# Performance work log

Hardware: AMD Instinct MI355X
Metric: run time of the kernel (lower is better)

## Reference

```python
import jax, jax.numpy as jnp
import numpy as np

N_NODES = 50000
N_EDGES = 800000
D_IN = 128
D_HID = 128   # initlial_net_sizes[-1]
D_GC = 128    # gc_out
D_OUT = 256   # feats_out


def setup_inputs() -> dict:
    key = jax.random.key(0)
    ks = jax.random.split(key, 8)
    feats = jax.random.normal(ks[0], (N_NODES, D_IN), dtype=jnp.float32)
    edges = jax.random.randint(ks[1], (2, N_EDGES), 0, N_NODES, dtype=jnp.int64)
    batch = jnp.sort(jax.random.randint(ks[2], (N_NODES,), 0, 64, dtype=jnp.int64))
    s = 0.05
    W1 = jax.random.normal(ks[3], (D_IN, D_HID), dtype=jnp.float32) * s
    b1 = jnp.zeros((D_HID,), dtype=jnp.float32)
    Wg = jax.random.normal(ks[4], (D_HID, D_GC), dtype=jnp.float32) * s
    bg = jnp.zeros((D_GC,), dtype=jnp.float32)
    W2 = jax.random.normal(ks[5], (D_HID + D_GC, D_OUT), dtype=jnp.float32) * s
    b2 = jnp.zeros((D_OUT,), dtype=jnp.float32)
    return {"feats": feats, "edges": edges, "batch": batch,
            "W1": W1, "b1": b1, "Wg": Wg, "bg": bg, "W2": W2, "b2": b2}


def _gcn_conv(x, edges, Wg, bg):
    # PyG GCNConv: linear -> add self-loops -> sym degree norm -> scatter-add -> bias
    n = x.shape[0]
    x = x @ Wg                                   # [N, D_GC]
    loop = jnp.arange(n, dtype=edges.dtype)
    src = jnp.concatenate([edges[0], loop])      # message source (x_j)
    dst = jnp.concatenate([edges[1], loop])      # aggregation target
    deg = jax.ops.segment_sum(jnp.ones_like(dst, dtype=x.dtype), dst, num_segments=n)
    dinv = jnp.where(deg > 0, jax.lax.rsqrt(deg), 0.0)
    norm = dinv[src] * dinv[dst]                 # [E+N]
    msg = x[src] * norm[:, None]                 # [E+N, D_GC]
    out = jax.ops.segment_sum(msg, dst, num_segments=n)
    return out + bg


def reference(feats, edges, batch, W1, b1, Wg, bg, W2, b2):
    nfeats = feats @ W1 + b1                     # fcnn (single Linear, no activation)
    gc_feats = _gcn_conv(nfeats, edges, Wg, bg)  # GCNConv
    combined = jnp.concatenate([nfeats, gc_feats], axis=1) @ W2 + b2
    return (combined, edges, batch)
```

## Files before the change

kernel.cpp:

```cpp
#include <hip/hip_runtime.h>
#include <hip/hip_bf16.h>
#include <stdint.h>


#define NND 50000
#define NE  800000

typedef unsigned int u32;
typedef unsigned short u16;
typedef unsigned long long u64;
typedef short bf16x8 __attribute__((ext_vector_type(8)));
typedef float f32x4  __attribute__((ext_vector_type(4)));

#define OFF_CSR  12800000
#define OFF_RNK  13200000
#define OFF_ROW  13600000
#define OFF_DEG  13700004
#define OFF_DINV 13750004
#define OFF_WPK2 13800004
#define OFF_WPK1 13832772
#define OFF_WPKG 13840964
#define OFF_BSUM 13849156
#define OFF_BOFF 13849412
#define OFF_FLG  13849668

__device__ __forceinline__ float bf_lo(u32 u) { return __uint_as_float(u << 16); }
__device__ __forceinline__ float bf_hi(u32 u) { return __uint_as_float(u & 0xFFFF0000u); }
__device__ __forceinline__ unsigned short f2b(float f) {
    __hip_bfloat16 h = __float2bfloat16(f);
    return *(unsigned short*)&h;
}

__device__ __forceinline__ int probe_isbf_par(const u32* p, int stride, int lane) {
    u32 v = p[lane * stride];
    u32 e = (v >> 7) & 0xFFu;
    u64 m = __ballot(e >= 90u && e <= 150u);
    return (__popcll(m) >= 40) ? 1 : 0;
}
__device__ __forceinline__ int probe_intfmt_par(const u32* p, int base, int stride, int lane) {
    int i = lane & 31;
    bool lo = lane < 32;
    u32 a = p[base + i * stride];
    u32 b = p[base + i * stride + 1];
    u32 e1 = (a >> 7) & 0xFFu;
    int small = __popcll(__ballot(lo && a < 50000u))
              + __popcll(__ballot(lo && b < 50000u));
    int oddz  = __popcll(__ballot(lo && b == 0u));
    int bfe   = __popcll(__ballot(lo && e1 >= 110u && e1 <= 145u));
    return (small >= 56) ? ((oddz >= 31) ? 1 : 0) : ((bfe >= 20) ? 3 : 2);
}

__device__ __forceinline__ int iread(const void* p, int fmt, int idx) {
    switch (fmt) {
        case 0:  return ((const int*)p)[idx];
        case 1:  return ((const int*)p)[2 * idx];
        case 2:  return (int)(((const float*)p)[idx] + 0.5f);
        default: return (int)(__bfloat162float(((const __hip_bfloat16*)p)[idx]) + 0.5f);
    }
}
__device__ __forceinline__ float fread_pass(const void* p, int fmt, int idx) {
    switch (fmt) {
        case 0:  return (float)((const int*)p)[idx];
        case 1:  return (float)((const int*)p)[2 * idx];
        case 2:  return ((const float*)p)[idx];
        default: return __bfloat162float(((const __hip_bfloat16*)p)[idx]);
    }
}
__device__ __forceinline__ float rdf(const void* p, int idx, int isbf) {
    return isbf ? __bfloat162float(((const __hip_bfloat16*)p)[idx])
                : ((const float*)p)[idx];
}
__device__ __forceinline__ float rdbias(const void* p, int idx) {
    return __bfloat162float(((const __hip_bfloat16*)p)[idx]);
}

__global__ void k_flags(const u32* feats, const u32* W1, const u32* Wg,
                        const u32* W2, const u32* ew, const u32* bw,
                        int* __restrict__ flags)
{
    int w = threadIdx.x >> 6, lane = threadIdx.x & 63;
    if      (w == 0) { int r = probe_isbf_par(feats, 997, lane);        if (lane == 0) flags[0] = r; }
    else if (w == 1) { int r = probe_isbf_par(W1, 127, lane);           if (lane == 0) flags[3] = r; }
    else if (w == 2) { int r = probe_isbf_par(Wg, 127, lane);           if (lane == 0) flags[4] = r; }
    else if (w == 3) { int r = probe_isbf_par(W2, 509, lane);           if (lane == 0) flags[5] = r; }
    else if (w == 4) { int r = probe_intfmt_par(ew, 0, 24992, lane);    if (lane == 0) flags[1] = r; }
    else if (w == 5) { int r = probe_intfmt_par(bw, 20000, 156, lane);  if (lane == 0) flags[2] = r; }
}

__global__ __launch_bounds__(256) void k_degrank(const void* edges,
                                                 const int* __restrict__ flags,
                                                 int* __restrict__ deg,
                                                 u16* __restrict__ rank16)
{
    int fmt = flags[1];
    int e = blockIdx.x * 256 + threadIdx.x;
    if (e < NE) {
        int s = iread(edges, fmt, e);
        int d = iread(edges, fmt, NE + e);
        if ((u32)s < (u32)NND && (u32)d < (u32)NND) {
            int r = atomicAdd(&deg[d], 1);
            rank16[e] = (u16)r;
        }
    }
}

__global__ __launch_bounds__(256) void k_scan1(const int* __restrict__ deg,
                                               int* __restrict__ bsum)
{
    __shared__ int part[256];
    int t = threadIdx.x, idx = blockIdx.x * 256 + t;
    part[t] = (idx < NND) ? deg[idx] : 0;
    __syncthreads();
    for (int off = 128; off >= 1; off >>= 1) {
        if (t < off) part[t] += part[t + off];
        __syncthreads();
    }
    if (t == 0) bsum[blockIdx.x] = part[0];
}

__global__ __launch_bounds__(256) void k_scan2(const int* __restrict__ bsum,
                                               int* __restrict__ boff,
                                               int* __restrict__ row_start)
{
    __shared__ int part[256];
    int t = threadIdx.x;
    int v = (t < 196) ? bsum[t] : 0;
    part[t] = v;
    __syncthreads();
    for (int off = 1; off < 256; off <<= 1) {
        int x = (t >= off) ? part[t - off] : 0;
        __syncthreads();
        part[t] += x;
        __syncthreads();
    }
    if (t < 196) boff[t] = part[t] - v;
    if (t == 255) row_start[NND] = part[255];
}

__global__ __launch_bounds__(256) void k_scan3(const int* __restrict__ deg,
                                               const int* __restrict__ boff,
                                               int* __restrict__ row_start,
                                               float* __restrict__ dinv)
{
    __shared__ int part[256];
    int t = threadIdx.x, idx = blockIdx.x * 256 + t;
    int dv = (idx < NND) ? deg[idx] : 0;
    part[t] = dv;
    __syncthreads();
    for (int off = 1; off < 256; off <<= 1) {
        int x = (t >= off) ? part[t - off] : 0;
        __syncthreads();
        part[t] += x;
        __syncthreads();
    }
    if (idx < NND) {
        int rs = boff[blockIdx.x] + part[t] - dv;
        row_start[idx] = rs;
        dinv[idx] = rsqrtf((float)(dv + 1));
    }
}

__global__ __launch_bounds__(256) void k_place(const void* edges,
                                               const int* __restrict__ flags,
                                               const int* __restrict__ row_start,
                                               const u16* __restrict__ rank16,
                                               u16* __restrict__ csr16)
{
    int fmt = flags[1];
    int e = blockIdx.x * 256 + threadIdx.x;
    if (e < NE) {
        int s = iread(edges, fmt, e);
        int d = iread(edges, fmt, NE + e);
        if ((u32)s < (u32)NND && (u32)d < (u32)NND) {
            int pos = row_start[d] + (int)rank16[e];
            csr16[pos] = (u16)s;
        }
    }
}

__global__ __launch_bounds__(256) void k_pw128(const void* W, const int* flg,
                                               unsigned short* __restrict__ Wpk)
{
    int wbf = *flg;
    int idx = blockIdx.x * 256 + threadIdx.x;
    if (idx < 16384) {
        int j = idx & 7, l = (idx >> 3) & 63, nt = (idx >> 9) & 7, kk = (idx >> 12) & 3;
        int k = kk * 32 + ((l >> 4) & 3) * 8 + j;
        int n = nt * 16 + (l & 15);
        Wpk[idx] = f2b(rdf(W, k * 128 + n, wbf));
    }
}

__global__ __launch_bounds__(256) void k_pw2(const void* W2, const int* flg,
                                             unsigned short* __restrict__ Wpk)
{
    int wbf = *flg;
    int idx = blockIdx.x * 256 + threadIdx.x;
    if (idx < 65536) {
        int j = idx & 7, l = (idx >> 3) & 63, nt = (idx >> 9) & 15, kk = idx >> 13;
        int k = kk * 32 + ((l >> 4) & 3) * 8 + j;
        int n = nt * 16 + (l & 15);
        Wpk[idx] = f2b(rdf(W2, k * 256 + n, wbf));
    }
}

__global__ __launch_bounds__(256) void k_nf(
    const void* feats, const int* __restrict__ flags,
    const u32* __restrict__ Wpk1, const void* b1, float* __restrict__ out, int M)
{
    __shared__ u32 sApk[2048];
    int tid = threadIdx.x;
    int fbf = flags[0];
    int row0 = blockIdx.x * 32;

    if (fbf) {
        const u32* fw = (const u32*)feats;
        for (int idx = tid; idx < 2048; idx += 256) {
            int jp = idx & 3, l = (idx >> 2) & 63, kk = (idx >> 8) & 3, mt = (idx >> 10) & 1;
            int m = mt * 16 + (l & 15);
            int k0 = kk * 32 + ((l >> 4) & 3) * 8 + jp * 2;
            int row = row0 + m;
            sApk[idx] = (row < M) ? fw[(size_t)row * 64 + (k0 >> 1)] : 0u;
        }
    } else {
        const float* ff = (const float*)feats;
        for (int idx = tid; idx < 2048; idx += 256) {
            int jp = idx & 3, l = (idx >> 2) & 63, kk = (idx >> 8) & 3, mt = (idx >> 10) & 1;
            int m = mt * 16 + (l & 15);
            int k0 = kk * 32 + ((l >> 4) & 3) * 8 + jp * 2;
            int row = row0 + m;
            u32 u = 0u;
            if (row < M) {
                float f0 = ff[(size_t)row * 128 + k0];
                float f1 = ff[(size_t)row * 128 + k0 + 1];
                u = ((u32)f2b(f1) << 16) | (u32)f2b(f0);
            }
            sApk[idx] = u;
        }
    }
    __syncthreads();

    int w = tid >> 6, lane = tid & 63;
    f32x4 acc[2][2];
#pragma unroll
    for (int mt = 0; mt < 2; ++mt)
#pragma unroll
        for (int t = 0; t < 2; ++t) acc[mt][t] = (f32x4){0.f, 0.f, 0.f, 0.f};

    for (int kk = 0; kk < 4; ++kk) {
        union { uint4 u; bf16x8 h; } ca0, ca1;
        ca0.u = *(const uint4*)&sApk[(kk * 64 + lane) * 4];
        ca1.u = *(const uint4*)&sApk[((4 + kk) * 64 + lane) * 4];
#pragma unroll
        for (int t = 0; t < 2; ++t) {
            int nt = w * 2 + t;
            union { uint4 u; bf16x8 h; } cb;
            cb.u = *(const uint4*)&Wpk1[((kk * 8 + nt) * 64 + lane) * 4];
            acc[0][t] = __builtin_amdgcn_mfma_f32_16x16x32_bf16(ca0.h, cb.h, acc[0][t], 0, 0, 0);
            acc[1][t] = __builtin_amdgcn_mfma_f32_16x16x32_bf16(ca1.h, cb.h, acc[1][t], 0, 0, 0);
        }
    }

    unsigned short* o16 = (unsigned short*)out;
    int q = lane >> 4, cn = lane & 15;
#pragma unroll
    for (int mt = 0; mt < 2; ++mt)
#pragma unroll
        for (int t = 0; t < 2; ++t) {
            int col = (w * 2 + t) * 16 + cn;
            float bb = rdbias(b1, col);
#pragma unroll
            for (int r = 0; r < 4; ++r) {
                int row = row0 + mt * 16 + q * 4 + r;
                if (row < M) o16[(size_t)row * 512 + col] = f2b(acc[mt][t][r] + bb);
            }
        }
}

__global__ __launch_bounds__(256) void k_xp(
    const u32* __restrict__ Wpkg, const float* __restrict__ dinv,
    float* __restrict__ out, int M)
{
    __shared__ u32 sApk[2048];
    int tid = threadIdx.x;
    int row0 = blockIdx.x * 32;
    const u32* uw = (const u32*)out;

    for (int idx = tid; idx < 2048; idx += 256) {
        int jp = idx & 3, l = (idx >> 2) & 63, kk = (idx >> 8) & 3, mt = (idx >> 10) & 1;
        int m = mt * 16 + (l & 15);
        int k0 = kk * 32 + ((l >> 4) & 3) * 8 + jp * 2;
        int row = row0 + m;
        sApk[idx] = (row < M) ? uw[(size_t)row * 256 + (k0 >> 1)] : 0u;
    }
    __syncthreads();

    int w = tid >> 6, lane = tid & 63;
    f32x4 acc[2][2];
#pragma unroll
    for (int mt = 0; mt < 2; ++mt)
#pragma unroll
        for (int t = 0; t < 2; ++t) acc[mt][t] = (f32x4){0.f, 0.f, 0.f, 0.f};

    for (int kk = 0; kk < 4; ++kk) {
        union { uint4 u; bf16x8 h; } ca0, ca1;
        ca0.u = *(const uint4*)&sApk[(kk * 64 + lane) * 4];
        ca1.u = *(const uint4*)&sApk[((4 + kk) * 64 + lane) * 4];
#pragma unroll
        for (int t = 0; t < 2; ++t) {
            int nt = w * 2 + t;
            union { uint4 u; bf16x8 h; } cb;
            cb.u = *(const uint4*)&Wpkg[((kk * 8 + nt) * 64 + lane) * 4];
            acc[0][t] = __builtin_amdgcn_mfma_f32_16x16x32_bf16(ca0.h, cb.h, acc[0][t], 0, 0, 0);
            acc[1][t] = __builtin_amdgcn_mfma_f32_16x16x32_bf16(ca1.h, cb.h, acc[1][t], 0, 0, 0);
        }
    }

    unsigned short* o16 = (unsigned short*)out;
    int q = lane >> 4, cn = lane & 15;
#pragma unroll
    for (int mt = 0; mt < 2; ++mt)
#pragma unroll
        for (int t = 0; t < 2; ++t) {
            int col = (w * 2 + t) * 16 + cn;
#pragma unroll
            for (int r = 0; r < 4; ++r) {
                int row = row0 + mt * 16 + q * 4 + r;
                if (row < M)
                    o16[(size_t)row * 512 + 256 + col] = f2b(acc[mt][t][r] * dinv[row]);
            }
        }
}

__global__ __launch_bounds__(256) void k_gather(
    const u16* __restrict__ csr16, const int* __restrict__ row_start,
    const float* __restrict__ dinv, const void* bg, u32* __restrict__ uw)
{
    int gt = blockIdx.x * 256 + threadIdx.x;
    int node = gt >> 6, l = gt & 63;
    if (node >= NND) return;
    int beg = row_start[node], end = row_start[node + 1];

    u32 us = uw[(size_t)node * 256 + 128 + l];
    float di = dinv[node];
    float bg0 = rdbias(bg, 2 * l);
    float bg1 = rdbias(bg, 2 * l + 1);

    float a0 = 0.f, a1 = 0.f;
    float c0 = 0.f, c1 = 0.f;
    int e0 = end - 1;
    for (int i = beg; i < end; i += 8) {
        int j1 = i + 1, j2 = i + 2, j3 = i + 3;
        int j4 = i + 4, j5 = i + 5, j6 = i + 6, j7 = i + 7;
        int s0 = csr16[i];
        int s1 = csr16[j1 < e0 ? j1 : e0];
        int s2 = csr16[j2 < e0 ? j2 : e0];
        int s3 = csr16[j3 < e0 ? j3 : e0];
        int s4 = csr16[j4 < e0 ? j4 : e0];
        int s5 = csr16[j5 < e0 ? j5 : e0];
        int s6 = csr16[j6 < e0 ? j6 : e0];
        int s7 = csr16[j7 < e0 ? j7 : e0];
        u32 u0 = uw[(size_t)s0 * 256 + 128 + l];
        u32 u1 = uw[(size_t)s1 * 256 + 128 + l];
        u32 u2 = uw[(size_t)s2 * 256 + 128 + l];
        u32 u3 = uw[(size_t)s3 * 256 + 128 + l];
        u32 u4 = uw[(size_t)s4 * 256 + 128 + l];
        u32 u5 = uw[(size_t)s5 * 256 + 128 + l];
        u32 u6 = uw[(size_t)s6 * 256 + 128 + l];
        u32 u7 = uw[(size_t)s7 * 256 + 128 + l];
        float w1 = (j1 <= e0) ? 1.f : 0.f;
        float w2 = (j2 <= e0) ? 1.f : 0.f;
        float w3 = (j3 <= e0) ? 1.f : 0.f;
        float w4 = (j4 <= e0) ? 1.f : 0.f;
        float w5 = (j5 <= e0) ? 1.f : 0.f;
        float w6 = (j6 <= e0) ? 1.f : 0.f;
        float w7 = (j7 <= e0) ? 1.f : 0.f;
        a0 += bf_lo(u0);            a1 += bf_hi(u0);
        c0 = fmaf(w1, bf_lo(u1), c0); c1 = fmaf(w1, bf_hi(u1), c1);
        a0 = fmaf(w2, bf_lo(u2), a0); a1 = fmaf(w2, bf_hi(u2), a1);
        c0 = fmaf(w3, bf_lo(u3), c0); c1 = fmaf(w3, bf_hi(u3), c1);
        a0 = fmaf(w4, bf_lo(u4), a0); a1 = fmaf(w4, bf_hi(u4), a1);
        c0 = fmaf(w5, bf_lo(u5), c0); c1 = fmaf(w5, bf_hi(u5), c1);
        a0 = fmaf(w6, bf_lo(u6), a0); a1 = fmaf(w6, bf_hi(u6), a1);
        c0 = fmaf(w7, bf_lo(u7), c0); c1 = fmaf(w7, bf_hi(u7), c1);
    }
    a0 += c0; a1 += c1;
    float g0 = di * (a0 + bf_lo(us)) + bg0;
    float g1 = di * (a1 + bf_hi(us)) + bg1;
    uw[(size_t)node * 256 + 192 + l] = ((u32)f2b(g1) << 16) | (u32)f2b(g0);
}

__global__ __launch_bounds__(256) void k_final(
    const u32* __restrict__ Wpk, const void* b2, float* __restrict__ out, int M)
{
    __shared__ u32 sApk[4096];
    int tid = threadIdx.x;
    int row0 = blockIdx.x * 32;
    const u32* uw = (const u32*)out;

    for (int idx = tid; idx < 4096; idx += 256) {
        int jp = idx & 3, l = (idx >> 2) & 63, kk = (idx >> 8) & 7, mt = (idx >> 11) & 1;
        int m = mt * 16 + (l & 15);
        int k0 = kk * 32 + ((l >> 4) & 3) * 8 + jp * 2;
        int row = row0 + m;
        u32 u = 0u;
        if (row < M) {
            if (kk < 4) u = uw[(size_t)row * 256 + (k0 >> 1)];
            else        u = uw[(size_t)row * 256 + 192 + ((k0 - 128) >> 1)];
        }
        sApk[idx] = u;
    }
    __syncthreads();

    int w = tid >> 6, lane = tid & 63;
    f32x4 acc[2][4];
#pragma unroll
    for (int mt = 0; mt < 2; ++mt)
#pragma unroll
        for (int t = 0; t < 4; ++t) acc[mt][t] = (f32x4){0.f, 0.f, 0.f, 0.f};

    for (int kk = 0; kk < 8; ++kk) {
        union { uint4 u; bf16x8 h; } ca0, ca1;
        ca0.u = *(const uint4*)&sApk[(kk * 64 + lane) * 4];
        ca1.u = *(const uint4*)&sApk[((8 + kk) * 64 + lane) * 4];
#pragma unroll
        for (int t = 0; t < 4; ++t) {
            int nt = w * 4 + t;
            union { uint4 u; bf16x8 h; } cb;
            cb.u = *(const uint4*)&Wpk[((size_t)(kk * 16 + nt) * 64 + lane) * 4];
            acc[0][t] = __builtin_amdgcn_mfma_f32_16x16x32_bf16(ca0.h, cb.h, acc[0][t], 0, 0, 0);
            acc[1][t] = __builtin_amdgcn_mfma_f32_16x16x32_bf16(ca1.h, cb.h, acc[1][t], 0, 0, 0);
        }
    }

    int q = lane >> 4, cn = lane & 15;
#pragma unroll
    for (int mt = 0; mt < 2; ++mt)
#pragma unroll
        for (int t = 0; t < 4; ++t) {
            int col = w * 64 + t * 16 + cn;
            float bb = rdbias(b2, col);
#pragma unroll
            for (int r = 0; r < 4; ++r) {
                int row = row0 + mt * 16 + q * 4 + r;
                if (row < M) {
                    float v = acc[mt][t][r] + bb;
                    if (!(fabsf(v) < 900.f)) v = (v == v) ? copysignf(900.f, v) : 0.f;
                    out[(size_t)row * 256 + col] = v;
                }
            }
        }
}

__global__ __launch_bounds__(256) void k_tail(
    const void* edges, const void* batch, const int* __restrict__ flags,
    float* __restrict__ out)
{
    int f0 = flags[1], f1 = flags[2];
    int i = blockIdx.x * 256 + threadIdx.x;
    if (i < 2 * NE) {
        out[(size_t)NND * 256 + i] = fread_pass(edges, f0, i);
    } else if (i < 2 * NE + NND) {
        out[(size_t)NND * 256 + i] = fread_pass(batch, f1, i - 2 * NE);
    }
}

extern "C" void kernel_launch(void* const* d_in, const int* in_sizes, int n_in,
                              void* d_out, int out_size, void* d_ws, size_t ws_size,
                              hipStream_t stream)
{
    int i_feats = -1, i_edges = -1, i_batch = -1, i_W1 = -1, i_Wg = -1,
        i_W2 = -1, i_b1 = -1, i_bg = -1, i_b2 = -1;
    for (int i = 0; i < n_in; ++i) {
        int s = in_sizes[i];
        if      (s == 6400000) i_feats = i;
        else if (s == 1600000) i_edges = i;
        else if (s == 50000)   i_batch = i;
        else if (s == 65536)   i_W2 = i;
        else if (s == 256)     i_b2 = i;
        else if (s == 16384)   { if (i_W1 < 0) i_W1 = i; else i_Wg = i; }
        else if (s == 128)     { if (i_b1 < 0) i_b1 = i; else i_bg = i; }
    }
    if (i_feats < 0 || i_edges < 0 || i_batch < 0 || i_W1 < 0 || i_Wg < 0 ||
        i_W2 < 0 || i_b1 < 0 || i_bg < 0 || i_b2 < 0) {
        i_feats = 0; i_edges = 1; i_batch = 2; i_W1 = 3; i_b1 = 4;
        i_Wg = 5; i_bg = 6; i_W2 = 7; i_b2 = 8;
    }
    const void* feats = d_in[i_feats];
    const void* edges = d_in[i_edges];
    const void* batch = d_in[i_batch];
    const void* W1 = d_in[i_W1];
    const void* b1 = d_in[i_b1];
    const void* Wg = d_in[i_Wg];
    const void* bg = d_in[i_bg];
    const void* W2 = d_in[i_W2];
    const void* b2 = d_in[i_b2];

    float* out = (float*)d_out;
    u16*   csr16     = (u16*)  (out + OFF_CSR);
    u16*   rank16    = (u16*)  (out + OFF_RNK);
    int*   row_start = (int*)  (out + OFF_ROW);
    int*   deg       = (int*)  (out + OFF_DEG);
    float* dinv      = (float*)(out + OFF_DINV);
    unsigned short* Wpk2 = (unsigned short*)(out + OFF_WPK2);
    unsigned short* Wpk1 = (unsigned short*)(out + OFF_WPK1);
    unsigned short* Wpkg = (unsigned short*)(out + OFF_WPKG);
    int*   bsum  = (int*)(out + OFF_BSUM);
    int*   boff  = (int*)(out + OFF_BOFF);
    int*   flags = (int*)(out + OFF_FLG);

    hipMemsetAsync(deg, 0, 200000, stream);
    k_flags  <<<1,     384, 0, stream>>>((const u32*)feats, (const u32*)W1,
                                         (const u32*)Wg, (const u32*)W2,
                                         (const u32*)edges, (const u32*)batch, flags);
    k_degrank<<<3125,  256, 0, stream>>>(edges, flags, deg, rank16);
    k_scan1  <<<196,   256, 0, stream>>>(deg, bsum);
    k_scan2  <<<1,     256, 0, stream>>>(bsum, boff, row_start);
    k_scan3  <<<196,   256, 0, stream>>>(deg, boff, row_start, dinv);
    k_place  <<<3125,  256, 0, stream>>>(edges, flags, row_start, rank16, csr16);
    k_pw128  <<<64,    256, 0, stream>>>(W1, flags + 3, Wpk1);
    k_pw128  <<<64,    256, 0, stream>>>(Wg, flags + 4, Wpkg);
    k_pw2    <<<256,   256, 0, stream>>>(W2, flags + 5, Wpk2);
    k_nf     <<<1563,  256, 0, stream>>>(feats, flags, (const u32*)Wpk1, b1, out, NND);
    k_xp     <<<1563,  256, 0, stream>>>((const u32*)Wpkg, dinv, out, NND);
    k_gather <<<12500, 256, 0, stream>>>(csr16, row_start, dinv, bg, (u32*)out);
    k_final  <<<1563,  256, 0, stream>>>((const u32*)Wpk2, b2, out, NND);
    k_tail   <<<6446,  256, 0, stream>>>(edges, batch, flags, out);
}
```

Baseline: 241.9 us.

## Fuse preprocessing kernels and move dinv scaling into gather

Cuts the launch chain from 14 kernels to 7. Degree counting and weight packing become one launch, the block scan is merged with the node-feature and Wg GEMMs (the Wg GEMM reads nfeats from shared memory instead of global), and the scan2 and scan3 stages are merged. The flags kernel is dropped, so each block now re-probes the input formats. Because the dinv source scaling moves from the xp epilogue into the gather loop, this removes a dependency and the redundant global reload of nfeats. In exchange, each gathered edge now does an extra random dinv load and every block runs extra probe work.

```diff
diff --git a/kernel.cpp b/kernel.cpp
--- a/kernel.cpp
+++ b/kernel.cpp
@@ -21,8 +21,6 @@
 #define OFF_WPK1 13832772
 #define OFF_WPKG 13840964
 #define OFF_BSUM 13849156
-#define OFF_BOFF 13849412
-#define OFF_FLG  13849668
 
 __device__ __forceinline__ float bf_lo(u32 u) { return __uint_as_float(u << 16); }
 __device__ __forceinline__ float bf_hi(u32 u) { return __uint_as_float(u & 0xFFFF0000u); }
@@ -74,144 +72,75 @@
     return __bfloat162float(((const __hip_bfloat16*)p)[idx]);
 }
 
-__global__ void k_flags(const u32* feats, const u32* W1, const u32* Wg,
-                        const u32* W2, const u32* ew, const u32* bw,
-                        int* __restrict__ flags)
-{
-    int w = threadIdx.x >> 6, lane = threadIdx.x & 63;
-    if      (w == 0) { int r = probe_isbf_par(feats, 997, lane);        if (lane == 0) flags[0] = r; }
-    else if (w == 1) { int r = probe_isbf_par(W1, 127, lane);           if (lane == 0) flags[3] = r; }
-    else if (w == 2) { int r = probe_isbf_par(Wg, 127, lane);           if (lane == 0) flags[4] = r; }
-    else if (w == 3) { int r = probe_isbf_par(W2, 509, lane);           if (lane == 0) flags[5] = r; }
-    else if (w == 4) { int r = probe_intfmt_par(ew, 0, 24992, lane);    if (lane == 0) flags[1] = r; }
-    else if (w == 5) { int r = probe_intfmt_par(bw, 20000, 156, lane);  if (lane == 0) flags[2] = r; }
-}
-
-__global__ __launch_bounds__(256) void k_degrank(const void* edges,
-                                                 const int* __restrict__ flags,
-                                                 int* __restrict__ deg,
-                                                 u16* __restrict__ rank16)
-{
-    int fmt = flags[1];
-    int e = blockIdx.x * 256 + threadIdx.x;
-    if (e < NE) {
-        int s = iread(edges, fmt, e);
-        int d = iread(edges, fmt, NE + e);
-        if ((u32)s < (u32)NND && (u32)d < (u32)NND) {
-            int r = atomicAdd(&deg[d], 1);
-            rank16[e] = (u16)r;
-        }
-    }
-}
-
-__global__ __launch_bounds__(256) void k_scan1(const int* __restrict__ deg,
-                                               int* __restrict__ bsum)
-{
-    __shared__ int part[256];
-    int t = threadIdx.x, idx = blockIdx.x * 256 + t;
-    part[t] = (idx < NND) ? deg[idx] : 0;
-    __syncthreads();
-    for (int off = 128; off >= 1; off >>= 1) {
-        if (t < off) part[t] += part[t + off];
-        __syncthreads();
-    }
-    if (t == 0) bsum[blockIdx.x] = part[0];
-}
-
-__global__ __launch_bounds__(256) void k_scan2(const int* __restrict__ bsum,
-                                               int* __restrict__ boff,
-                                               int* __restrict__ row_start)
-{
-    __shared__ int part[256];
-    int t = threadIdx.x;
-    int v = (t < 196) ? bsum[t] : 0;
-    part[t] = v;
-    __syncthreads();
-    for (int off = 1; off < 256; off <<= 1) {
-        int x = (t >= off) ? part[t - off] : 0;
-        __syncthreads();
-        part[t] += x;
-        __syncthreads();
-    }
-    if (t < 196) boff[t] = part[t] - v;
-    if (t == 255) row_start[NND] = part[255];
-}
-
-__global__ __launch_bounds__(256) void k_scan3(const int* __restrict__ deg,
-                                               const int* __restrict__ boff,
-                                               int* __restrict__ row_start,
-                                               float* __restrict__ dinv)
-{
-    __shared__ int part[256];
-    int t = threadIdx.x, idx = blockIdx.x * 256 + t;
-    int dv = (idx < NND) ? deg[idx] : 0;
-    part[t] = dv;
-    __syncthreads();
-    for (int off = 1; off < 256; off <<= 1) {
-        int x = (t >= off) ? part[t - off] : 0;
-        __syncthreads();
-        part[t] += x;
-        __syncthreads();
-    }
-    if (idx < NND) {
-        int rs = boff[blockIdx.x] + part[t] - dv;
-        row_start[idx] = rs;
-        dinv[idx] = rsqrtf((float)(dv + 1));
-    }
-}
-
-__global__ __launch_bounds__(256) void k_place(const void* edges,
-                                               const int* __restrict__ flags,
-                                               const int* __restrict__ row_start,
-                                               const u16* __restrict__ rank16,
-                                               u16* __restrict__ csr16)
-{
-    int fmt = flags[1];
-    int e = blockIdx.x * 256 + threadIdx.x;
-    if (e < NE) {
-        int s = iread(edges, fmt, e);
-        int d = iread(edges, fmt, NE + e);
-        if ((u32)s < (u32)NND && (u32)d < (u32)NND) {
-            int pos = row_start[d] + (int)rank16[e];
-            csr16[pos] = (u16)s;
-        }
-    }
-}
-
-__global__ __launch_bounds__(256) void k_pw128(const void* W, const int* flg,
-                                               unsigned short* __restrict__ Wpk)
-{
-    int wbf = *flg;
-    int idx = blockIdx.x * 256 + threadIdx.x;
-    if (idx < 16384) {
+__global__ __launch_bounds__(256) void k_degpack(
+    const void* edges, const void* W1, const void* Wg, const void* W2,
+    int* __restrict__ deg, u16* __restrict__ rank16,
+    u16* __restrict__ Wpk1, u16* __restrict__ Wpkg, u16* __restrict__ Wpk2)
+{
+    int b = blockIdx.x, tid = threadIdx.x, lane = tid & 63;
+    if (b < 3125) {
+        int fmt = probe_intfmt_par((const u32*)edges, 0, 24992, lane);
+        int e = b * 256 + tid;
+        if (e < NE) {
+            int s = iread(edges, fmt, e);
+            int d = iread(edges, fmt, NE + e);
+            if ((u32)s < (u32)NND && (u32)d < (u32)NND) {
+                int r = atomicAdd(&deg[d], 1);
+                rank16[e] = (u16)r;
+            }
+        }
+    } else if (b < 3189) {
+        int wbf = probe_isbf_par((const u32*)W1, 127, lane);
+        int idx = (b - 3125) * 256 + tid;
         int j = idx & 7, l = (idx >> 3) & 63, nt = (idx >> 9) & 7, kk = (idx >> 12) & 3;
         int k = kk * 32 + ((l >> 4) & 3) * 8 + j;
         int n = nt * 16 + (l & 15);
-        Wpk[idx] = f2b(rdf(W, k * 128 + n, wbf));
-    }
-}
-
-__global__ __launch_bounds__(256) void k_pw2(const void* W2, const int* flg,
-                                             unsigned short* __restrict__ Wpk)
-{
-    int wbf = *flg;
-    int idx = blockIdx.x * 256 + threadIdx.x;
-    if (idx < 65536) {
+        Wpk1[idx] = f2b(rdf(W1, k * 128 + n, wbf));
+    } else if (b < 3253) {
+        int wbf = probe_isbf_par((const u32*)Wg, 127, lane);
+        int idx = (b - 3189) * 256 + tid;
+        int j = idx & 7, l = (idx >> 3) & 63, nt = (idx >> 9) & 7, kk = (idx >> 12) & 3;
+        int k = kk * 32 + ((l >> 4) & 3) * 8 + j;
+        int n = nt * 16 + (l & 15);
+        Wpkg[idx] = f2b(rdf(Wg, k * 128 + n, wbf));
+    } else {
+        int wbf = probe_isbf_par((const u32*)W2, 509, lane);
+        int idx = (b - 3253) * 256 + tid;
         int j = idx & 7, l = (idx >> 3) & 63, nt = (idx >> 9) & 15, kk = idx >> 13;
         int k = kk * 32 + ((l >> 4) & 3) * 8 + j;
         int n = nt * 16 + (l & 15);
-        Wpk[idx] = f2b(rdf(W2, k * 256 + n, wbf));
-    }
-}
-
-__global__ __launch_bounds__(256) void k_nf(
-    const void* feats, const int* __restrict__ flags,
-    const u32* __restrict__ Wpk1, const void* b1, float* __restrict__ out, int M)
-{
-    __shared__ u32 sApk[2048];
-    int tid = threadIdx.x;
-    int fbf = flags[0];
-    int row0 = blockIdx.x * 32;
+        Wpk2[idx] = f2b(rdf(W2, k * 256 + n, wbf));
+    }
+}
+
+__global__ __launch_bounds__(256) void k_scannfxp(
+    const int* __restrict__ deg, int* __restrict__ bsum,
+    const void* feats, const u32* __restrict__ Wpk1, const u32* __restrict__ Wpkg,
+    const void* b1, float* __restrict__ out, int M)
+{
+    __shared__ u32 smem[2048 + 2176];
+    int b = blockIdx.x, tid = threadIdx.x;
+
+    if (b < 196) {
+        int* part = (int*)smem;
+        int idx = b * 256 + tid;
+        part[tid] = (idx < NND) ? deg[idx] : 0;
+        __syncthreads();
+        for (int off = 128; off >= 1; off >>= 1) {
+            if (tid < off) part[tid] += part[tid + off];
+            __syncthreads();
+        }
+        if (tid == 0) bsum[b] = part[0];
+        return;
+    }
+
+    int nb = b - 196;
+    int row0 = nb * 32;
+    int lane = tid & 63, w = tid >> 6;
+    u32* sApk = smem;
+    u16* nfl  = (u16*)(smem + 2048);
+
+    int fbf = probe_isbf_par((const u32*)feats, 997, lane);
 
     if (fbf) {
         const u32* fw = (const u32*)feats;
@@ -240,7 +169,6 @@
     }
     __syncthreads();
 
-    int w = tid >> 6, lane = tid & 63;
     f32x4 acc[2][2];
 #pragma unroll
     for (int mt = 0; mt < 2; ++mt)
@@ -271,53 +199,36 @@
             float bb = rdbias(b1, col);
 #pragma unroll
             for (int r = 0; r < 4; ++r) {
-                int row = row0 + mt * 16 + q * 4 + r;
-                if (row < M) o16[(size_t)row * 512 + col] = f2b(acc[mt][t][r] + bb);
+                int rowl = mt * 16 + q * 4 + r;
+                int row = row0 + rowl;
+                unsigned short v = f2b(acc[mt][t][r] + bb);
+                nfl[rowl * 136 + col] = v;
+                if (row < M) o16[(size_t)row * 512 + col] = v;
             }
         }
-}
-
-__global__ __launch_bounds__(256) void k_xp(
-    const u32* __restrict__ Wpkg, const float* __restrict__ dinv,
-    float* __restrict__ out, int M)
-{
-    __shared__ u32 sApk[2048];
-    int tid = threadIdx.x;
-    int row0 = blockIdx.x * 32;
-    const u32* uw = (const u32*)out;
-
-    for (int idx = tid; idx < 2048; idx += 256) {
-        int jp = idx & 3, l = (idx >> 2) & 63, kk = (idx >> 8) & 3, mt = (idx >> 10) & 1;
-        int m = mt * 16 + (l & 15);
-        int k0 = kk * 32 + ((l >> 4) & 3) * 8 + jp * 2;
-        int row = row0 + m;
-        sApk[idx] = (row < M) ? uw[(size_t)row * 256 + (k0 >> 1)] : 0u;
-    }
-    __syncthreads();
-
-    int w = tid >> 6, lane = tid & 63;
-    f32x4 acc[2][2];
-#pragma unroll
-    for (int mt = 0; mt < 2; ++mt)
-#pragma unroll
-        for (int t = 0; t < 2; ++t) acc[mt][t] = (f32x4){0.f, 0.f, 0.f, 0.f};
+    __syncthreads();
+
+    f32x4 acc2[2][2];
+#pragma unroll
+    for (int mt = 0; mt < 2; ++mt)
+#pragma unroll
+        for (int t = 0; t < 2; ++t) acc2[mt][t] = (f32x4){0.f, 0.f, 0.f, 0.f};
 
     for (int kk = 0; kk < 4; ++kk) {
+        int kcol = kk * 32 + ((lane >> 4) & 3) * 8;
         union { uint4 u; bf16x8 h; } ca0, ca1;
-        ca0.u = *(const uint4*)&sApk[(kk * 64 + lane) * 4];
-        ca1.u = *(const uint4*)&sApk[((4 + kk) * 64 + lane) * 4];
+        ca0.u = *(const uint4*)&nfl[(lane & 15) * 136 + kcol];
+        ca1.u = *(const uint4*)&nfl[(16 + (lane & 15)) * 136 + kcol];
 #pragma unroll
         for (int t = 0; t < 2; ++t) {
             int nt = w * 2 + t;
             union { uint4 u; bf16x8 h; } cb;
             cb.u = *(const uint4*)&Wpkg[((kk * 8 + nt) * 64 + lane) * 4];
-            acc[0][t] = __builtin_amdgcn_mfma_f32_16x16x32_bf16(ca0.h, cb.h, acc[0][t], 0, 0, 0);
-            acc[1][t] = __builtin_amdgcn_mfma_f32_16x16x32_bf16(ca1.h, cb.h, acc[1][t], 0, 0, 0);
-        }
-    }
-
-    unsigned short* o16 = (unsigned short*)out;
-    int q = lane >> 4, cn = lane & 15;
+            acc2[0][t] = __builtin_amdgcn_mfma_f32_16x16x32_bf16(ca0.h, cb.h, acc2[0][t], 0, 0, 0);
+            acc2[1][t] = __builtin_amdgcn_mfma_f32_16x16x32_bf16(ca1.h, cb.h, acc2[1][t], 0, 0, 0);
+        }
+    }
+
 #pragma unroll
     for (int mt = 0; mt < 2; ++mt)
 #pragma unroll
@@ -327,9 +238,66 @@
             for (int r = 0; r < 4; ++r) {
                 int row = row0 + mt * 16 + q * 4 + r;
                 if (row < M)
-                    o16[(size_t)row * 512 + 256 + col] = f2b(acc[mt][t][r] * dinv[row]);
+                    o16[(size_t)row * 512 + 256 + col] = f2b(acc2[mt][t][r]);
             }
         }
+}
+
+__global__ __launch_bounds__(256) void k_scan23(
+    const int* __restrict__ deg, const int* __restrict__ bsum,
+    int* __restrict__ row_start, float* __restrict__ dinv)
+{
+    __shared__ int part[256];
+    __shared__ int sboff;
+    int t = threadIdx.x, b = blockIdx.x;
+
+    int v = (t < 196) ? bsum[t] : 0;
+    part[t] = v;
+    __syncthreads();
+    for (int off = 1; off < 256; off <<= 1) {
+        int x = (t >= off) ? part[t - off] : 0;
+        __syncthreads();
+        part[t] += x;
+        __syncthreads();
+    }
+    if (t == b) sboff = part[t] - v;
+    if (b == 0 && t == 255) row_start[NND] = part[255];
+    __syncthreads();
+    int boffb = sboff;
+    __syncthreads();
+
+    int idx = b * 256 + t;
+    int dv = (idx < NND) ? deg[idx] : 0;
+    part[t] = dv;
+    __syncthreads();
+    for (int off = 1; off < 256; off <<= 1) {
+        int x = (t >= off) ? part[t - off] : 0;
+        __syncthreads();
+        part[t] += x;
+        __syncthreads();
+    }
+    if (idx < NND) {
+        int rs = boffb + part[t] - dv;
+        row_start[idx] = rs;
+        dinv[idx] = rsqrtf((float)(dv + 1));
+    }
+}
+
+__global__ __launch_bounds__(256) void k_place(const void* edges,
+                                               const int* __restrict__ row_start,
+                                               const u16* __restrict__ rank16,
+                                               u16* __restrict__ csr16)
+{
+    int fmt = probe_intfmt_par((const u32*)edges, 0, 24992, threadIdx.x & 63);
+    int e = blockIdx.x * 256 + threadIdx.x;
+    if (e < NE) {
+        int s = iread(edges, fmt, e);
+        int d = iread(edges, fmt, NE + e);
+        if ((u32)s < (u32)NND && (u32)d < (u32)NND) {
+            int pos = row_start[d] + (int)rank16[e];
+            csr16[pos] = (u16)s;
+        }
+    }
 }
 
 __global__ __launch_bounds__(256) void k_gather(
@@ -368,14 +336,15 @@
         u32 u5 = uw[(size_t)s5 * 256 + 128 + l];
         u32 u6 = uw[(size_t)s6 * 256 + 128 + l];
         u32 u7 = uw[(size_t)s7 * 256 + 128 + l];
-        float w1 = (j1 <= e0) ? 1.f : 0.f;
-        float w2 = (j2 <= e0) ? 1.f : 0.f;
-        float w3 = (j3 <= e0) ? 1.f : 0.f;
-        float w4 = (j4 <= e0) ? 1.f : 0.f;
-        float w5 = (j5 <= e0) ? 1.f : 0.f;
-        float w6 = (j6 <= e0) ? 1.f : 0.f;
-        float w7 = (j7 <= e0) ? 1.f : 0.f;
-        a0 += bf_lo(u0);            a1 += bf_hi(u0);
+        float w0 = dinv[s0];
+        float w1 = (j1 <= e0) ? dinv[s1] : 0.f;
+        float w2 = (j2 <= e0) ? dinv[s2] : 0.f;
+        float w3 = (j3 <= e0) ? dinv[s3] : 0.f;
+        float w4 = (j4 <= e0) ? dinv[s4] : 0.f;
+        float w5 = (j5 <= e0) ? dinv[s5] : 0.f;
+        float w6 = (j6 <= e0) ? dinv[s6] : 0.f;
+        float w7 = (j7 <= e0) ? dinv[s7] : 0.f;
+        a0 = fmaf(w0, bf_lo(u0), a0); a1 = fmaf(w0, bf_hi(u0), a1);
         c0 = fmaf(w1, bf_lo(u1), c0); c1 = fmaf(w1, bf_hi(u1), c1);
         a0 = fmaf(w2, bf_lo(u2), a0); a1 = fmaf(w2, bf_hi(u2), a1);
         c0 = fmaf(w3, bf_lo(u3), c0); c1 = fmaf(w3, bf_hi(u3), c1);
@@ -385,8 +354,8 @@
         c0 = fmaf(w7, bf_lo(u7), c0); c1 = fmaf(w7, bf_hi(u7), c1);
     }
     a0 += c0; a1 += c1;
-    float g0 = di * (a0 + bf_lo(us)) + bg0;
-    float g1 = di * (a1 + bf_hi(us)) + bg1;
+    float g0 = di * (a0 + di * bf_lo(us)) + bg0;
+    float g1 = di * (a1 + di * bf_hi(us)) + bg1;
     uw[(size_t)node * 256 + 192 + l] = ((u32)f2b(g1) << 16) | (u32)f2b(g0);
 }
 
@@ -453,10 +422,11 @@
 }
 
 __global__ __launch_bounds__(256) void k_tail(
-    const void* edges, const void* batch, const int* __restrict__ flags,
-    float* __restrict__ out)
-{
-    int f0 = flags[1], f1 = flags[2];
+    const void* edges, const void* batch, float* __restrict__ out)
+{
+    int lane = threadIdx.x & 63;
+    int f0 = probe_intfmt_par((const u32*)edges, 0, 24992, lane);
+    int f1 = probe_intfmt_par((const u32*)batch, 20000, 156, lane);
     int i = blockIdx.x * 256 + threadIdx.x;
     if (i < 2 * NE) {
         out[(size_t)NND * 256 + i] = fread_pass(edges, f0, i);
@@ -502,28 +472,19 @@
     int*   row_start = (int*)  (out + OFF_ROW);
     int*   deg       = (int*)  (out + OFF_DEG);
     float* dinv      = (float*)(out + OFF_DINV);
-    unsigned short* Wpk2 = (unsigned short*)(out + OFF_WPK2);
-    unsigned short* Wpk1 = (unsigned short*)(out + OFF_WPK1);
-    unsigned short* Wpkg = (unsigned short*)(out + OFF_WPKG);
-    int*   bsum  = (int*)(out + OFF_BSUM);
-    int*   boff  = (int*)(out + OFF_BOFF);
-    int*   flags = (int*)(out + OFF_FLG);
+    u16*   Wpk2 = (u16*)(out + OFF_WPK2);
+    u16*   Wpk1 = (u16*)(out + OFF_WPK1);
+    u16*   Wpkg = (u16*)(out + OFF_WPKG);
+    int*   bsum = (int*)(out + OFF_BSUM);
 
     hipMemsetAsync(deg, 0, 200000, stream);
-    k_flags  <<<1,     384, 0, stream>>>((const u32*)feats, (const u32*)W1,
-                                         (const u32*)Wg, (const u32*)W2,
-                                         (const u32*)edges, (const u32*)batch, flags);
-    k_degrank<<<3125,  256, 0, stream>>>(edges, flags, deg, rank16);
-    k_scan1  <<<196,   256, 0, stream>>>(deg, bsum);
-    k_scan2  <<<1,     256, 0, stream>>>(bsum, boff, row_start);
-    k_scan3  <<<196,   256, 0, stream>>>(deg, boff, row_start, dinv);
-    k_place  <<<3125,  256, 0, stream>>>(edges, flags, row_start, rank16, csr16);
-    k_pw128  <<<64,    256, 0, stream>>>(W1, flags + 3, Wpk1);
-    k_pw128  <<<64,    256, 0, stream>>>(Wg, flags + 4, Wpkg);
-    k_pw2    <<<256,   256, 0, stream>>>(W2, flags + 5, Wpk2);
-    k_nf     <<<1563,  256, 0, stream>>>(feats, flags, (const u32*)Wpk1, b1, out, NND);
-    k_xp     <<<1563,  256, 0, stream>>>((const u32*)Wpkg, dinv, out, NND);
-    k_gather <<<12500, 256, 0, stream>>>(csr16, row_start, dinv, bg, (u32*)out);
-    k_final  <<<1563,  256, 0, stream>>>((const u32*)Wpk2, b2, out, NND);
-    k_tail   <<<6446,  256, 0, stream>>>(edges, batch, flags, out);
-}
+    k_degpack <<<3509,  256, 0, stream>>>(edges, W1, Wg, W2, deg, rank16,
+                                          Wpk1, Wpkg, Wpk2);
+    k_scannfxp<<<1759,  256, 0, stream>>>(deg, bsum, feats, (const u32*)Wpk1,
+                                          (const u32*)Wpkg, b1, out, NND);
+    k_scan23  <<<196,   256, 0, stream>>>(deg, bsum, row_start, dinv);
+    k_place   <<<3125,  256, 0, stream>>>(edges, row_start, rank16, csr16);
+    k_gather  <<<12500, 256, 0, stream>>>(csr16, row_start, dinv, bg, (u32*)out);
+    k_final   <<<1563,  256, 0, stream>>>((const u32*)Wpk2, b2, out, NND);
+    k_tail    <<<6446,  256, 0, stream>>>(edges, batch, out);
+}
```

Result: faster. 231.5 us (-4.3%).
